# Performance work log

Hardware: AMD Instinct MI355X
Metric: run time of the kernel (lower is better)

The kernel has to match this reference:

```python
import jax, jax.numpy as jnp
import numpy as np

N, E, B = 50000, 800000, 1000
NODE_DIN, BB_DOUT, DHID, K = 32, 64, 64, 3
GLOB_DIN, EMBED_DIN = 64, 64
CIN = BB_DOUT + NODE_DIN  # 96


def setup_inputs() -> dict:
    key = jax.random.key(0)
    ks = jax.random.split(key, 24)

    def w(k, shape, fan_in):
        return jax.random.normal(k, shape, jnp.float32) / np.float32(np.sqrt(fan_in))

    inp = dict(
        x=jax.random.normal(ks[0], (N, NODE_DIN), jnp.float32),
        u=jax.random.normal(ks[1], (B, GLOB_DIN), jnp.float32),
        z=jax.random.normal(ks[2], (N, BB_DOUT), jnp.float32),
        edge_index=jax.random.randint(ks[3], (2, E), 0, N),
        edge_weight=jax.random.uniform(ks[4], (E,), jnp.float32),
        batch=jnp.sort(jax.random.randint(ks[5], (N,), 0, B)),
        batch_size=B,
        prev_h=jax.random.normal(ks[6], (N, DHID), jnp.float32),
    )
    # six ChebConvs of GConvGRU: x-convs take CIN, h-convs take DHID; all output DHID
    for i, nm in enumerate(["xz", "hz", "xr", "hr", "xh", "hh"]):
        cin = CIN if nm[0] == "x" else DHID
        inp[f"W{nm}"] = w(ks[7 + 2 * i], (K, cin, DHID), cin * K)
        inp[f"b{nm}"] = jnp.zeros((DHID,), jnp.float32)
    inp["Wg"] = w(ks[20], (GLOB_DIN, EMBED_DIN), GLOB_DIN)
    inp["bg"] = jnp.zeros((EMBED_DIN,), jnp.float32)
    return inp


def _cheb(xin, W, b, src, dst, w_norm, n):
    """ChebConv with sym norm, lambda_max=2 -> L_hat = -D^-1/2 A D^-1/2 (diag cancels)."""
    def prop(t):  # L_hat @ t  ([N,C])
        return -jax.ops.segment_sum(w_norm[:, None] * t[src], dst, num_segments=n)

    out = xin @ W[0] + b
    tx_prev = xin
    tx = None
    if W.shape[0] > 1:
        tx = prop(xin)
        out = out + tx @ W[1]
    for k in range(2, W.shape[0]):
        tx_new = 2.0 * prop(tx) - tx_prev
        out = out + tx_new @ W[k]
        tx_prev, tx = tx, tx_new
    return out


def reference(x, u, z, edge_index, edge_weight, batch, batch_size, prev_h,
              Wxz, bxz, Whz, bhz, Wxr, bxr, Whr, bhr, Wxh, bxh, Whh, bhh, Wg, bg):
    n = x.shape[0]
    src, dst = edge_index[0], edge_index[1]
    deg = jax.ops.segment_sum(edge_weight, src, num_segments=n)
    deg_safe = jnp.where(deg > 0, deg, 1.0)
    dinv = jnp.where(deg > 0, jax.lax.rsqrt(deg_safe), 0.0)
    w_norm = dinv[src] * edge_weight * dinv[dst]

    xin = jnp.concatenate([z, x], axis=-1)  # [N, CIN]
    Z = jax.nn.sigmoid(_cheb(xin, Wxz, bxz, src, dst, w_norm, n)
                       + _cheb(prev_h, Whz, bhz, src, dst, w_norm, n))
    R = jax.nn.sigmoid(_cheb(xin, Wxr, bxr, src, dst, w_norm, n)
                       + _cheb(prev_h, Whr, bhr, src, dst, w_norm, n))
    Ht = jnp.tanh(_cheb(xin, Wxh, bxh, src, dst, w_norm, n)
                  + _cheb(prev_h * R, Whh, bhh, src, dst, w_norm, n))
    h = Z * prev_h + (1.0 - Z) * Ht

    graph_emb = jax.ops.segment_sum(z, batch, num_segments=batch_size)  # [B, BB_DOUT]
    global_emb = jax.nn.relu(u @ Wg + bg)                                # [B, EMBED_DIN]
    fused = jnp.concatenate([graph_emb, global_emb], axis=-1)           # [B, 128]
    return fused, h
```

## Files before the change

kernel.cpp:

```cpp
#include <hip/hip_runtime.h>

#define NN 50000
#define EE 800000
#define BB 1000
#define NB 196
#define NR 8
#define RS 6272
#define NC 32
#define CHUNK 25000

typedef unsigned short u16;
typedef __attribute__((ext_vector_type(8))) short bf16x8;
typedef __attribute__((ext_vector_type(4))) float f32x4;

static __device__ __forceinline__ u16 f2b(float f) {
    union { float f; unsigned u; } v;
    v.f = f;
    unsigned r = v.u + 0x7fffu + ((v.u >> 16) & 1u);
    return (u16)(r >> 16);
}

static __device__ __forceinline__ float b2f(short s) {
    union { unsigned u; float f; } c;
    c.u = ((unsigned)(u16)s) << 16;
    return c.f;
}

__global__ __launch_bounds__(512) void k_degcnt_lds(
    const int* __restrict__ src, const int* __restrict__ dst,
    const float* __restrict__ ew, float* __restrict__ deg_p,
    int* __restrict__ cnt_p) {
    __shared__ float sdeg[RS];
    __shared__ int scnt[RS];
    int r = blockIdx.x & (NR - 1);
    int c = blockIdx.x >> 3;
    int base = r * RS;
    for (int i = threadIdx.x; i < RS; i += 512) {
        sdeg[i] = 0.f;
        scnt[i] = 0;
    }
    __syncthreads();
    int e0 = c * CHUNK;
    for (int j = threadIdx.x; j < CHUNK; j += 512) {
        int e = e0 + j;
        int s = src[e], d = dst[e];
        int sl = s - base, dl = d - base;
        if ((unsigned)sl < RS) atomicAdd(&sdeg[sl], ew[e]);
        if ((unsigned)dl < RS) atomicAdd(&scnt[dl], 1);
    }
    __syncthreads();
    int lim = (NN - base < RS) ? (NN - base) : RS;
    for (int i = threadIdx.x; i < lim; i += 512) {
        deg_p[(size_t)c * NN + base + i] = sdeg[i];
        cnt_p[(size_t)c * NN + base + i] = scnt[i];
    }
}

__global__ void k_scan1(const int* __restrict__ cnt_p, int* __restrict__ cnt,
                        int* __restrict__ incl, int* __restrict__ bsum) {
    __shared__ int s[256];
    int i = blockIdx.x * 256 + threadIdx.x;
    int v = 0;
    if (i < NN) {
#pragma unroll
        for (int p = 0; p < NC; p++) v += cnt_p[(size_t)p * NN + i];
        cnt[i] = v;
    }
    s[threadIdx.x] = v;
    __syncthreads();
    for (int off = 1; off < 256; off <<= 1) {
        int t = (threadIdx.x >= off) ? s[threadIdx.x - off] : 0;
        __syncthreads();
        s[threadIdx.x] += t;
        __syncthreads();
    }
    if (i < NN) incl[i] = s[threadIdx.x];
    if (threadIdx.x == 255) bsum[blockIdx.x] = s[255];
}

__global__ void k_scan2(int* __restrict__ bsum) {
    __shared__ int s[256];
    int v = (threadIdx.x < NB) ? bsum[threadIdx.x] : 0;
    s[threadIdx.x] = v;
    __syncthreads();
    for (int off = 1; off < 256; off <<= 1) {
        int t = (threadIdx.x >= off) ? s[threadIdx.x - off] : 0;
        __syncthreads();
        s[threadIdx.x] += t;
        __syncthreads();
    }
    if (threadIdx.x < NB) bsum[threadIdx.x] = s[threadIdx.x];
}

__global__ void k_scan3(const int* __restrict__ incl, const int* __restrict__ cnt,
                        const int* __restrict__ bsum, int* __restrict__ row_ptr,
                        int* __restrict__ cursor, const float* __restrict__ deg_p,
                        float* __restrict__ dinv) {
    int i = blockIdx.x * 256 + threadIdx.x;
    if (i >= NN) return;
    int off = (blockIdx.x > 0) ? bsum[blockIdx.x - 1] : 0;
    int start = off + incl[i] - cnt[i];
    row_ptr[i] = start;
    cursor[i] = start;
    float d = 0.f;
#pragma unroll
    for (int p = 0; p < NC; p++) d += deg_p[(size_t)p * NN + i];
    dinv[i] = d > 0.f ? rsqrtf(d) : 0.f;
}

__global__ void k_scatter(const int* __restrict__ src, const int* __restrict__ dst,
                          const float* __restrict__ ew, const float* __restrict__ dinv,
                          int* __restrict__ cursor, uint2* __restrict__ csr8) {
    int e = blockIdx.x * 256 + threadIdx.x;
    if (e >= EE) return;
    int d = dst[e], s = src[e];
    int pos = atomicAdd(&cursor[d], 1);
    float w = dinv[s] * ew[e] * dinv[d];
    csr8[pos] = make_uint2((unsigned)s, __float_as_uint(w));
}

__global__ void k_build_A(const float* __restrict__ z, const float* __restrict__ x,
                          const float* __restrict__ ph, u16* __restrict__ A) {
    int i = blockIdx.x * 256 + threadIdx.x;
    if (i >= NN * 160) return;
    int n = i / 160, c = i - n * 160;
    float v;
    if (c < 64) v = z[n * 64 + c];
    else if (c < 96) v = x[n * 32 + (c - 64)];
    else v = ph[n * 64 + (c - 96)];
    A[(size_t)n * 480 + c] = f2b(v);
}

__global__ void k_packW_all(const float* __restrict__ Wxz, const float* __restrict__ Wxr,
                            const float* __restrict__ Wxh, const float* __restrict__ Whz,
                            const float* __restrict__ Whr, const float* __restrict__ Whh,
                            u16* __restrict__ Wp, u16* __restrict__ W3p) {
    int idx = blockIdx.x * 256 + threadIdx.x;
    if (idx < 15 * 12 * 512) {
        int j = idx & 7, l = (idx >> 3) & 63;
        int ct = (idx >> 9) % 12, s = (idx >> 9) / 12;
        int k = 32 * s + (l >> 4) * 8 + j;
        int g = ct >> 2;
        int c = 16 * (ct & 3) + (l & 15);
        bool isX;
        int kr;
        if (k < 96)       { isX = true;  kr = k; }
        else if (k < 160) { isX = false; kr = k - 96; }
        else if (k < 256) { isX = true;  kr = 96 + (k - 160); }
        else if (k < 320) { isX = false; kr = 64 + (k - 256); }
        else if (k < 416) { isX = true;  kr = 192 + (k - 320); }
        else              { isX = false; kr = 128 + (k - 416); }
        float val;
        if (isX) {
            const float* W = (g == 0) ? Wxz : ((g == 1) ? Wxr : Wxh);
            val = W[kr * 64 + c];
        } else if (g == 2) {
            val = 0.f;
        } else {
            const float* W = (g == 0) ? Whz : Whr;
            val = W[kr * 64 + c];
        }
        Wp[idx] = f2b(val);
    } else {
        int i2 = idx - 15 * 12 * 512;
        if (i2 >= 6 * 4 * 512) return;
        int j = i2 & 7, l = (i2 >> 3) & 63;
        int ct = (i2 >> 9) & 3, s = i2 >> 11;
        int k = 32 * s + (l >> 4) * 8 + j;
        int ki = k >> 6, kr = k & 63;
        int c = 16 * ct + (l & 15);
        W3p[i2] = f2b(Whh[(ki * 64 + kr) * 64 + c]);
    }
}

template <int C, int SCALE, bool HB, int BS, int OS>
__global__ __launch_bounds__(BS) void k_pull(
    const u16* __restrict__ Abase, int inofs, int baseofs, int outofs,
    const uint2* __restrict__ csr8, const int* __restrict__ row_ptr,
    const int* __restrict__ cnt) {
    constexpr int TPR = C / 8;
    int tid = blockIdx.x * BS + threadIdx.x;
    int r = tid / TPR;
    int c8 = (tid - r * TPR) * 8;
    if (r >= NN) return;
    int s0 = row_ptr[r], n = cnt[r];
    float acc[8] = {0.f, 0.f, 0.f, 0.f, 0.f, 0.f, 0.f, 0.f};
    const u16* in = Abase + inofs + c8;
    uint2 e = (n > 0) ? csr8[s0] : make_uint2(0u, 0u);
    for (int j = 0; j < n; j++) {
        uint2 ec = e;
        if (j + 1 < n) e = csr8[s0 + j + 1];
        float w = __uint_as_float(ec.y);
        bf16x8 v = *(const bf16x8*)(in + (size_t)ec.x * OS);
#pragma unroll
        for (int k = 0; k < 8; k++) acc[k] += w * b2f(v[k]);
    }
    const float sc = -(float)SCALE;
    float o[8];
    if (HB) {
        bf16x8 b = *(const bf16x8*)(Abase + (size_t)r * OS + baseofs + c8);
#pragma unroll
        for (int k = 0; k < 8; k++) o[k] = sc * acc[k] - b2f(b[k]);
    } else {
#pragma unroll
        for (int k = 0; k < 8; k++) o[k] = sc * acc[k];
    }
    bf16x8 p;
#pragma unroll
    for (int k = 0; k < 8; k++) p[k] = (short)f2b(o[k]);
    *(bf16x8*)(const_cast<u16*>(Abase) + (size_t)r * OS + outofs + c8) = p;
}

__global__ __launch_bounds__(256) void k_gates_mfma(
    const u16* __restrict__ A, const u16* __restrict__ Wp,
    const float* __restrict__ bxz, const float* __restrict__ bhz,
    const float* __restrict__ bxr, const float* __restrict__ bhr,
    const float* __restrict__ bxh,
    u16* __restrict__ Zb16, u16* __restrict__ Hx16, u16* __restrict__ A3) {
    int wv = (blockIdx.x * 256 + threadIdx.x) >> 6;
    int lane = threadIdx.x & 63;
    int r0 = wv * 16;
    if (r0 >= NN) return;
    int q = lane >> 4, j0 = lane & 15;

    f32x4 acc[12];
#pragma unroll
    for (int i = 0; i < 12; i++) acc[i] = (f32x4){0.f, 0.f, 0.f, 0.f};

    const u16* arow = A + (size_t)(r0 + j0) * 480 + q * 8;
#pragma unroll
    for (int s = 0; s < 15; s++) {
        bf16x8 a = *(const bf16x8*)(arow + 32 * s);
        const u16* bp = Wp + (size_t)(s * 12) * 512 + lane * 8;
#pragma unroll
        for (int ct = 0; ct < 12; ct++) {
            bf16x8 b = *(const bf16x8*)(bp + ct * 512);
            acc[ct] = __builtin_amdgcn_mfma_f32_16x16x32_bf16(a, b, acc[ct], 0, 0, 0);
        }
    }

#pragma unroll
    for (int ct = 0; ct < 4; ct++) {
        int j = 16 * ct + j0;
        float bz = bxz[j] + bhz[j];
        float br = bxr[j] + bhr[j];
        float bh = bxh[j];
#pragma unroll
        for (int reg = 0; reg < 4; reg++) {
            int r = r0 + q * 4 + reg;
            size_t i = (size_t)r * 64 + j;
            float zp = acc[ct][reg] + bz;
            float rp = acc[ct + 4][reg] + br;
            float hp = acc[ct + 8][reg] + bh;
            float zv = 1.f / (1.f + expf(-zp));
            float rv = 1.f / (1.f + expf(-rp));
            float phv = b2f((short)A[(size_t)r * 480 + 96 + j]);
            Zb16[i] = f2b(zv);
            Hx16[i] = f2b(hp);
            A3[(size_t)r * 192 + j] = f2b(rv * phv);
        }
    }
}

__global__ __launch_bounds__(256) void k_final_mfma(
    const u16* __restrict__ A3, const u16* __restrict__ W3p,
    const float* __restrict__ bhh, const u16* __restrict__ Hx16,
    const u16* __restrict__ Zb16, const u16* __restrict__ A,
    float* __restrict__ outh) {
    int wv = (blockIdx.x * 256 + threadIdx.x) >> 6;
    int lane = threadIdx.x & 63;
    int r0 = wv * 16;
    if (r0 >= NN) return;
    int q = lane >> 4, j0 = lane & 15;

    f32x4 acc[4];
#pragma unroll
    for (int i = 0; i < 4; i++) acc[i] = (f32x4){0.f, 0.f, 0.f, 0.f};

    const u16* arow = A3 + (size_t)(r0 + j0) * 192 + q * 8;
#pragma unroll
    for (int s = 0; s < 6; s++) {
        bf16x8 a = *(const bf16x8*)(arow + 32 * s);
        const u16* bp = W3p + (size_t)(s * 4) * 512 + lane * 8;
#pragma unroll
        for (int ct = 0; ct < 4; ct++) {
            bf16x8 b = *(const bf16x8*)(bp + ct * 512);
            acc[ct] = __builtin_amdgcn_mfma_f32_16x16x32_bf16(a, b, acc[ct], 0, 0, 0);
        }
    }

#pragma unroll
    for (int ct = 0; ct < 4; ct++) {
        int j = 16 * ct + j0;
        float bh = bhh[j];
#pragma unroll
        for (int reg = 0; reg < 4; reg++) {
            int r = r0 + q * 4 + reg;
            size_t i = (size_t)r * 64 + j;
            float ht = tanhf(b2f((short)Hx16[i]) + acc[ct][reg] + bh);
            float zv = b2f((short)Zb16[i]);
            float phv = b2f((short)A[(size_t)r * 480 + 96 + j]);
            outh[i] = zv * phv + (1.f - zv) * ht;
        }
    }
}

__global__ __launch_bounds__(256) void k_tail(
    const float* __restrict__ z, const int* __restrict__ batch,
    const float* __restrict__ u, const float* __restrict__ Wg,
    const float* __restrict__ bg, float* __restrict__ out) {
    int b = (blockIdx.x * 256 + threadIdx.x) >> 6;
    int lane = threadIdx.x & 63;
    if (b >= BB) return;
    int lo = 0, hi = NN;
    while (lo < hi) {
        int m = (lo + hi) >> 1;
        if (batch[m] < b) lo = m + 1; else hi = m;
    }
    int start = lo;
    hi = NN;
    while (lo < hi) {
        int m = (lo + hi) >> 1;
        if (batch[m] < b + 1) lo = m + 1; else hi = m;
    }
    int end = lo;
    float acc = 0.f;
    for (int n = start; n < end; n++) acc += z[(size_t)n * 64 + lane];
    float g = bg[lane];
    const float* ur = u + (size_t)b * 64;
    for (int k = 0; k < 64; k++) g += ur[k] * Wg[k * 64 + lane];
    g = fmaxf(g, 0.f);
    out[(size_t)b * 128 + lane] = acc;
    out[(size_t)b * 128 + 64 + lane] = g;
}

extern "C" void kernel_launch(void* const* d_in, const int* in_sizes, int n_in,
                              void* d_out, int out_size, void* d_ws, size_t ws_size,
                              hipStream_t stream) {
    const float* x  = (const float*)d_in[0];
    const float* u  = (const float*)d_in[1];
    const float* z  = (const float*)d_in[2];
    const int*   ei = (const int*)d_in[3];
    const float* ew = (const float*)d_in[4];
    const int* batch = (const int*)d_in[5];
    const float* ph = (const float*)d_in[7];
    const float *Wxz = (const float*)d_in[8],  *bxz = (const float*)d_in[9];
    const float *Whz = (const float*)d_in[10], *bhz = (const float*)d_in[11];
    const float *Wxr = (const float*)d_in[12], *bxr = (const float*)d_in[13];
    const float *Whr = (const float*)d_in[14], *bhr = (const float*)d_in[15];
    const float *Wxh = (const float*)d_in[16], *bxh = (const float*)d_in[17];
    const float *Whh = (const float*)d_in[18], *bhh = (const float*)d_in[19];
    const float *Wg  = (const float*)d_in[20], *bg  = (const float*)d_in[21];
    const int* src = ei;
    const int* dst = ei + EE;

    char* wsb = (char*)d_ws;
    size_t o = 0;
    auto alloc = [&](size_t bytes) {
        void* p = wsb + o;
        o += (bytes + 255) & ~(size_t)255;
        return p;
    };
    float* deg_p   = (float*)alloc((size_t)NC * NN * 4);
    int*   cnt_p   = (int*)alloc((size_t)NC * NN * 4);
    int*   cnt     = (int*)alloc(NN * 4);
    int*   incl    = (int*)alloc(NN * 4);
    int*   row_ptr = (int*)alloc(NN * 4);
    int*   cursor  = (int*)alloc(NN * 4);
    float* dinv    = (float*)alloc(NN * 4);
    int*   bsum    = (int*)alloc(256 * 4);
    uint2* csr8    = (uint2*)alloc((size_t)EE * 8);
    u16*   Zb16 = (u16*)alloc((size_t)NN * 64 * 2);
    u16*   Hx16 = (u16*)alloc((size_t)NN * 64 * 2);
    u16*   A    = (u16*)alloc((size_t)NN * 480 * 2);
    u16*   A3   = (u16*)alloc((size_t)NN * 192 * 2);
    u16*   Wp   = (u16*)alloc(15 * 12 * 512 * 2);
    u16*   W3p  = (u16*)alloc(6 * 4 * 512 * 2);

    float* outF = (float*)d_out;
    float* outH = outF + (size_t)BB * 128;

    const int BLK = 256;
    const int gE = (EE + BLK - 1) / BLK;
    const int gA = (NN * 160 + BLK - 1) / BLK;
    const int gPull160 = (NN + 15) / 16;
    const int gPull64 = (NN + 31) / 32;
    const int gMFMA = (3125 + 3) / 4;
    const int gPack = (15 * 12 * 512 + 6 * 4 * 512 + BLK - 1) / BLK;

    k_packW_all<<<gPack, BLK, 0, stream>>>(Wxz, Wxr, Wxh, Whz, Whr, Whh, Wp, W3p);
    k_build_A<<<gA, BLK, 0, stream>>>(z, x, ph, A);

    k_degcnt_lds<<<NR * NC, 512, 0, stream>>>(src, dst, ew, deg_p, cnt_p);

    k_scan1<<<NB, 256, 0, stream>>>(cnt_p, cnt, incl, bsum);
    k_scan2<<<1, 256, 0, stream>>>(bsum);
    k_scan3<<<NB, 256, 0, stream>>>(incl, cnt, bsum, row_ptr, cursor, deg_p, dinv);
    k_scatter<<<gE, BLK, 0, stream>>>(src, dst, ew, dinv, cursor, csr8);

    k_pull<160, 1, false, 320, 480><<<gPull160, 320, 0, stream>>>(A, 0, 0, 160, csr8, row_ptr, cnt);
    k_pull<160, 2, true, 320, 480><<<gPull160, 320, 0, stream>>>(A, 160, 0, 320, csr8, row_ptr, cnt);

    k_gates_mfma<<<gMFMA, BLK, 0, stream>>>(A, Wp, bxz, bhz, bxr, bhr, bxh, Zb16, Hx16, A3);

    k_pull<64, 1, false, 256, 192><<<gPull64, 256, 0, stream>>>(A3, 0, 0, 64, csr8, row_ptr, cnt);
    k_pull<64, 2, true, 256, 192><<<gPull64, 256, 0, stream>>>(A3, 64, 0, 128, csr8, row_ptr, cnt);

    k_final_mfma<<<gMFMA, BLK, 0, stream>>>(A3, W3p, bhh, Hx16, Zb16, A, outH);

    k_tail<<<(BB * 64 + BLK - 1) / BLK, BLK, 0, stream>>>(z, batch, u, Wg, bg, outF);
}
```

Baseline: 425.7 us.

## Merge prep kernels, fuse scan passes with grid barrier, widen pull per-thread columns

```diff
diff --git a/kernel.cpp b/kernel.cpp
--- a/kernel.cpp
+++ b/kernel.cpp
@@ -9,6 +9,10 @@
 #define NC 32
 #define CHUNK 25000
 
+#define DEGBLKS (NR * NC)
+#define BUILDBLKS 15625
+#define PACKBLKS 204
+
 typedef unsigned short u16;
 typedef __attribute__((ext_vector_type(8))) short bf16x8;
 typedef __attribute__((ext_vector_type(4))) float f32x4;
@@ -26,44 +30,103 @@
     return c.f;
 }
 
-__global__ __launch_bounds__(512) void k_degcnt_lds(
+__global__ __launch_bounds__(512) void k_front(
     const int* __restrict__ src, const int* __restrict__ dst,
-    const float* __restrict__ ew, float* __restrict__ deg_p,
-    int* __restrict__ cnt_p) {
+    const float* __restrict__ ew, float* __restrict__ deg_p, int* __restrict__ cnt_p,
+    const float* __restrict__ z, const float* __restrict__ x,
+    const float* __restrict__ ph, u16* __restrict__ A,
+    const float* __restrict__ Wxz, const float* __restrict__ Wxr,
+    const float* __restrict__ Wxh, const float* __restrict__ Whz,
+    const float* __restrict__ Whr, const float* __restrict__ Whh,
+    u16* __restrict__ Wp, u16* __restrict__ W3p, int* __restrict__ ctr) {
     __shared__ float sdeg[RS];
     __shared__ int scnt[RS];
-    int r = blockIdx.x & (NR - 1);
-    int c = blockIdx.x >> 3;
-    int base = r * RS;
-    for (int i = threadIdx.x; i < RS; i += 512) {
-        sdeg[i] = 0.f;
-        scnt[i] = 0;
-    }
-    __syncthreads();
-    int e0 = c * CHUNK;
-    for (int j = threadIdx.x; j < CHUNK; j += 512) {
-        int e = e0 + j;
-        int s = src[e], d = dst[e];
-        int sl = s - base, dl = d - base;
-        if ((unsigned)sl < RS) atomicAdd(&sdeg[sl], ew[e]);
-        if ((unsigned)dl < RS) atomicAdd(&scnt[dl], 1);
-    }
-    __syncthreads();
-    int lim = (NN - base < RS) ? (NN - base) : RS;
-    for (int i = threadIdx.x; i < lim; i += 512) {
-        deg_p[(size_t)c * NN + base + i] = sdeg[i];
-        cnt_p[(size_t)c * NN + base + i] = scnt[i];
-    }
-}
-
-__global__ void k_scan1(const int* __restrict__ cnt_p, int* __restrict__ cnt,
-                        int* __restrict__ incl, int* __restrict__ bsum) {
+    int bid = blockIdx.x;
+    if (bid < DEGBLKS) {
+        if (bid == 0 && threadIdx.x == 0) atomicExch(ctr, 0);
+        int r = bid & (NR - 1);
+        int c = bid >> 3;
+        int base = r * RS;
+        for (int i = threadIdx.x; i < RS; i += 512) {
+            sdeg[i] = 0.f;
+            scnt[i] = 0;
+        }
+        __syncthreads();
+        int e0 = c * CHUNK;
+        for (int j = threadIdx.x; j < CHUNK; j += 512) {
+            int e = e0 + j;
+            int s = src[e], d = dst[e];
+            int sl = s - base, dl = d - base;
+            if ((unsigned)sl < RS) atomicAdd(&sdeg[sl], ew[e]);
+            if ((unsigned)dl < RS) atomicAdd(&scnt[dl], 1);
+        }
+        __syncthreads();
+        int lim = (NN - base < RS) ? (NN - base) : RS;
+        for (int i = threadIdx.x; i < lim; i += 512) {
+            deg_p[(size_t)c * NN + base + i] = sdeg[i];
+            cnt_p[(size_t)c * NN + base + i] = scnt[i];
+        }
+    } else if (bid < DEGBLKS + BUILDBLKS) {
+        int i = (bid - DEGBLKS) * 512 + threadIdx.x;
+        int n = i / 160, c = i - n * 160;
+        float v;
+        if (c < 64) v = z[n * 64 + c];
+        else if (c < 96) v = x[n * 32 + (c - 64)];
+        else v = ph[n * 64 + (c - 96)];
+        A[(size_t)n * 480 + c] = f2b(v);
+    } else {
+        int idx = (bid - DEGBLKS - BUILDBLKS) * 512 + threadIdx.x;
+        if (idx < 15 * 12 * 512) {
+            int j = idx & 7, l = (idx >> 3) & 63;
+            int ct = (idx >> 9) % 12, s = (idx >> 9) / 12;
+            int k = 32 * s + (l >> 4) * 8 + j;
+            int g = ct >> 2;
+            int c = 16 * (ct & 3) + (l & 15);
+            bool isX;
+            int kr;
+            if (k < 96)       { isX = true;  kr = k; }
+            else if (k < 160) { isX = false; kr = k - 96; }
+            else if (k < 256) { isX = true;  kr = 96 + (k - 160); }
+            else if (k < 320) { isX = false; kr = 64 + (k - 256); }
+            else if (k < 416) { isX = true;  kr = 192 + (k - 320); }
+            else              { isX = false; kr = 128 + (k - 416); }
+            float val;
+            if (isX) {
+                const float* W = (g == 0) ? Wxz : ((g == 1) ? Wxr : Wxh);
+                val = W[kr * 64 + c];
+            } else if (g == 2) {
+                val = 0.f;
+            } else {
+                const float* W = (g == 0) ? Whz : Whr;
+                val = W[kr * 64 + c];
+            }
+            Wp[idx] = f2b(val);
+        } else {
+            int i2 = idx - 15 * 12 * 512;
+            int j = i2 & 7, l = (i2 >> 3) & 63;
+            int ct = (i2 >> 9) & 3, s = i2 >> 11;
+            int k = 32 * s + (l >> 4) * 8 + j;
+            int ki = k >> 6, kr = k & 63;
+            int c = 16 * ct + (l & 15);
+            W3p[i2] = f2b(Whh[(ki * 64 + kr) * 64 + c]);
+        }
+    }
+}
+
+__global__ __launch_bounds__(256) void k_scan(
+    const int* __restrict__ cnt_p, const float* __restrict__ deg_p,
+    int* __restrict__ cnt, int* __restrict__ row_ptr, int* __restrict__ cursor,
+    float* __restrict__ dinv, int* __restrict__ bsum, int* __restrict__ ctr) {
     __shared__ int s[256];
-    int i = blockIdx.x * 256 + threadIdx.x;
+    int b = blockIdx.x;
+    int i = b * 256 + threadIdx.x;
     int v = 0;
+    float d = 0.f;
     if (i < NN) {
 #pragma unroll
         for (int p = 0; p < NC; p++) v += cnt_p[(size_t)p * NN + i];
+#pragma unroll
+        for (int p = 0; p < NC; p++) d += deg_p[(size_t)p * NN + i];
         cnt[i] = v;
     }
     s[threadIdx.x] = v;
@@ -74,38 +137,29 @@
         s[threadIdx.x] += t;
         __syncthreads();
     }
-    if (i < NN) incl[i] = s[threadIdx.x];
-    if (threadIdx.x == 255) bsum[blockIdx.x] = s[255];
-}
-
-__global__ void k_scan2(int* __restrict__ bsum) {
-    __shared__ int s[256];
-    int v = (threadIdx.x < NB) ? bsum[threadIdx.x] : 0;
-    s[threadIdx.x] = v;
+    int incl = s[threadIdx.x];
+    if (threadIdx.x == 255) atomicExch(&bsum[b], s[255]);
+    __threadfence();
+    if (threadIdx.x == 0) {
+        atomicAdd(ctr, 1);
+        while (atomicAdd(ctr, 0) < NB) __builtin_amdgcn_s_sleep(8);
+    }
     __syncthreads();
-    for (int off = 1; off < 256; off <<= 1) {
-        int t = (threadIdx.x >= off) ? s[threadIdx.x - off] : 0;
+    __threadfence();
+    int pv = (threadIdx.x < b) ? atomicAdd(&bsum[threadIdx.x], 0) : 0;
+    s[threadIdx.x] = pv;
+    __syncthreads();
+    for (int off = 128; off > 0; off >>= 1) {
+        if (threadIdx.x < off) s[threadIdx.x] += s[threadIdx.x + off];
         __syncthreads();
-        s[threadIdx.x] += t;
-        __syncthreads();
-    }
-    if (threadIdx.x < NB) bsum[threadIdx.x] = s[threadIdx.x];
-}
-
-__global__ void k_scan3(const int* __restrict__ incl, const int* __restrict__ cnt,
-                        const int* __restrict__ bsum, int* __restrict__ row_ptr,
-                        int* __restrict__ cursor, const float* __restrict__ deg_p,
-                        float* __restrict__ dinv) {
-    int i = blockIdx.x * 256 + threadIdx.x;
-    if (i >= NN) return;
-    int off = (blockIdx.x > 0) ? bsum[blockIdx.x - 1] : 0;
-    int start = off + incl[i] - cnt[i];
-    row_ptr[i] = start;
-    cursor[i] = start;
-    float d = 0.f;
-#pragma unroll
-    for (int p = 0; p < NC; p++) d += deg_p[(size_t)p * NN + i];
-    dinv[i] = d > 0.f ? rsqrtf(d) : 0.f;
+    }
+    int prefix = s[0];
+    if (i < NN) {
+        int start = prefix + incl - v;
+        row_ptr[i] = start;
+        cursor[i] = start;
+        dinv[i] = d > 0.f ? rsqrtf(d) : 0.f;
+    }
 }
 
 __global__ void k_scatter(const int* __restrict__ src, const int* __restrict__ dst,
@@ -119,96 +173,59 @@
     csr8[pos] = make_uint2((unsigned)s, __float_as_uint(w));
 }
 
-__global__ void k_build_A(const float* __restrict__ z, const float* __restrict__ x,
-                          const float* __restrict__ ph, u16* __restrict__ A) {
-    int i = blockIdx.x * 256 + threadIdx.x;
-    if (i >= NN * 160) return;
-    int n = i / 160, c = i - n * 160;
-    float v;
-    if (c < 64) v = z[n * 64 + c];
-    else if (c < 96) v = x[n * 32 + (c - 64)];
-    else v = ph[n * 64 + (c - 96)];
-    A[(size_t)n * 480 + c] = f2b(v);
-}
-
-__global__ void k_packW_all(const float* __restrict__ Wxz, const float* __restrict__ Wxr,
-                            const float* __restrict__ Wxh, const float* __restrict__ Whz,
-                            const float* __restrict__ Whr, const float* __restrict__ Whh,
-                            u16* __restrict__ Wp, u16* __restrict__ W3p) {
-    int idx = blockIdx.x * 256 + threadIdx.x;
-    if (idx < 15 * 12 * 512) {
-        int j = idx & 7, l = (idx >> 3) & 63;
-        int ct = (idx >> 9) % 12, s = (idx >> 9) / 12;
-        int k = 32 * s + (l >> 4) * 8 + j;
-        int g = ct >> 2;
-        int c = 16 * (ct & 3) + (l & 15);
-        bool isX;
-        int kr;
-        if (k < 96)       { isX = true;  kr = k; }
-        else if (k < 160) { isX = false; kr = k - 96; }
-        else if (k < 256) { isX = true;  kr = 96 + (k - 160); }
-        else if (k < 320) { isX = false; kr = 64 + (k - 256); }
-        else if (k < 416) { isX = true;  kr = 192 + (k - 320); }
-        else              { isX = false; kr = 128 + (k - 416); }
-        float val;
-        if (isX) {
-            const float* W = (g == 0) ? Wxz : ((g == 1) ? Wxr : Wxh);
-            val = W[kr * 64 + c];
-        } else if (g == 2) {
-            val = 0.f;
-        } else {
-            const float* W = (g == 0) ? Whz : Whr;
-            val = W[kr * 64 + c];
-        }
-        Wp[idx] = f2b(val);
-    } else {
-        int i2 = idx - 15 * 12 * 512;
-        if (i2 >= 6 * 4 * 512) return;
-        int j = i2 & 7, l = (i2 >> 3) & 63;
-        int ct = (i2 >> 9) & 3, s = i2 >> 11;
-        int k = 32 * s + (l >> 4) * 8 + j;
-        int ki = k >> 6, kr = k & 63;
-        int c = 16 * ct + (l & 15);
-        W3p[i2] = f2b(Whh[(ki * 64 + kr) * 64 + c]);
-    }
-}
-
 template <int C, int SCALE, bool HB, int BS, int OS>
 __global__ __launch_bounds__(BS) void k_pull(
     const u16* __restrict__ Abase, int inofs, int baseofs, int outofs,
     const uint2* __restrict__ csr8, const int* __restrict__ row_ptr,
     const int* __restrict__ cnt) {
-    constexpr int TPR = C / 8;
+    constexpr int TPR = C / 16;
     int tid = blockIdx.x * BS + threadIdx.x;
     int r = tid / TPR;
-    int c8 = (tid - r * TPR) * 8;
+    int c16 = (tid - r * TPR) * 16;
     if (r >= NN) return;
     int s0 = row_ptr[r], n = cnt[r];
-    float acc[8] = {0.f, 0.f, 0.f, 0.f, 0.f, 0.f, 0.f, 0.f};
-    const u16* in = Abase + inofs + c8;
+    float acc[16];
+#pragma unroll
+    for (int k = 0; k < 16; k++) acc[k] = 0.f;
+    const u16* in = Abase + inofs + c16;
     uint2 e = (n > 0) ? csr8[s0] : make_uint2(0u, 0u);
     for (int j = 0; j < n; j++) {
         uint2 ec = e;
         if (j + 1 < n) e = csr8[s0 + j + 1];
         float w = __uint_as_float(ec.y);
-        bf16x8 v = *(const bf16x8*)(in + (size_t)ec.x * OS);
-#pragma unroll
-        for (int k = 0; k < 8; k++) acc[k] += w * b2f(v[k]);
+        const u16* p = in + (size_t)ec.x * OS;
+        bf16x8 v0 = *(const bf16x8*)(p);
+        bf16x8 v1 = *(const bf16x8*)(p + 8);
+#pragma unroll
+        for (int k = 0; k < 8; k++) {
+            acc[k] += w * b2f(v0[k]);
+            acc[8 + k] += w * b2f(v1[k]);
+        }
     }
     const float sc = -(float)SCALE;
-    float o[8];
+    float o[16];
     if (HB) {
-        bf16x8 b = *(const bf16x8*)(Abase + (size_t)r * OS + baseofs + c8);
-#pragma unroll
-        for (int k = 0; k < 8; k++) o[k] = sc * acc[k] - b2f(b[k]);
+        const u16* bp = Abase + (size_t)r * OS + baseofs + c16;
+        bf16x8 b0 = *(const bf16x8*)(bp);
+        bf16x8 b1 = *(const bf16x8*)(bp + 8);
+#pragma unroll
+        for (int k = 0; k < 8; k++) {
+            o[k] = sc * acc[k] - b2f(b0[k]);
+            o[8 + k] = sc * acc[8 + k] - b2f(b1[k]);
+        }
     } else {
 #pragma unroll
-        for (int k = 0; k < 8; k++) o[k] = sc * acc[k];
-    }
-    bf16x8 p;
-#pragma unroll
-    for (int k = 0; k < 8; k++) p[k] = (short)f2b(o[k]);
-    *(bf16x8*)(const_cast<u16*>(Abase) + (size_t)r * OS + outofs + c8) = p;
+        for (int k = 0; k < 16; k++) o[k] = sc * acc[k];
+    }
+    bf16x8 p0, p1;
+#pragma unroll
+    for (int k = 0; k < 8; k++) {
+        p0[k] = (short)f2b(o[k]);
+        p1[k] = (short)f2b(o[8 + k]);
+    }
+    u16* op = const_cast<u16*>(Abase) + (size_t)r * OS + outofs + c16;
+    *(bf16x8*)(op) = p0;
+    *(bf16x8*)(op + 8) = p1;
 }
 
 __global__ __launch_bounds__(256) void k_gates_mfma(
@@ -262,11 +279,41 @@
     }
 }
 
-__global__ __launch_bounds__(256) void k_final_mfma(
+#define FINBLKS 782
+__global__ __launch_bounds__(256) void k_final_tail(
     const u16* __restrict__ A3, const u16* __restrict__ W3p,
     const float* __restrict__ bhh, const u16* __restrict__ Hx16,
     const u16* __restrict__ Zb16, const u16* __restrict__ A,
-    float* __restrict__ outh) {
+    float* __restrict__ outh,
+    const float* __restrict__ z, const int* __restrict__ batch,
+    const float* __restrict__ u, const float* __restrict__ Wg,
+    const float* __restrict__ bg, float* __restrict__ outF) {
+    if (blockIdx.x >= FINBLKS) {
+        int b = ((blockIdx.x - FINBLKS) * 256 + threadIdx.x) >> 6;
+        int lane = threadIdx.x & 63;
+        if (b >= BB) return;
+        int lo = 0, hi = NN;
+        while (lo < hi) {
+            int m = (lo + hi) >> 1;
+            if (batch[m] < b) lo = m + 1; else hi = m;
+        }
+        int start = lo;
+        hi = NN;
+        while (lo < hi) {
+            int m = (lo + hi) >> 1;
+            if (batch[m] < b + 1) lo = m + 1; else hi = m;
+        }
+        int end = lo;
+        float acc = 0.f;
+        for (int n = start; n < end; n++) acc += z[(size_t)n * 64 + lane];
+        float g = bg[lane];
+        const float* ur = u + (size_t)b * 64;
+        for (int k = 0; k < 64; k++) g += ur[k] * Wg[k * 64 + lane];
+        g = fmaxf(g, 0.f);
+        outF[(size_t)b * 128 + lane] = acc;
+        outF[(size_t)b * 128 + 64 + lane] = g;
+        return;
+    }
     int wv = (blockIdx.x * 256 + threadIdx.x) >> 6;
     int lane = threadIdx.x & 63;
     int r0 = wv * 16;
@@ -303,35 +350,6 @@
             outh[i] = zv * phv + (1.f - zv) * ht;
         }
     }
-}
-
-__global__ __launch_bounds__(256) void k_tail(
-    const float* __restrict__ z, const int* __restrict__ batch,
-    const float* __restrict__ u, const float* __restrict__ Wg,
-    const float* __restrict__ bg, float* __restrict__ out) {
-    int b = (blockIdx.x * 256 + threadIdx.x) >> 6;
-    int lane = threadIdx.x & 63;
-    if (b >= BB) return;
-    int lo = 0, hi = NN;
-    while (lo < hi) {
-        int m = (lo + hi) >> 1;
-        if (batch[m] < b) lo = m + 1; else hi = m;
-    }
-    int start = lo;
-    hi = NN;
-    while (lo < hi) {
-        int m = (lo + hi) >> 1;
-        if (batch[m] < b + 1) lo = m + 1; else hi = m;
-    }
-    int end = lo;
-    float acc = 0.f;
-    for (int n = start; n < end; n++) acc += z[(size_t)n * 64 + lane];
-    float g = bg[lane];
-    const float* ur = u + (size_t)b * 64;
-    for (int k = 0; k < 64; k++) g += ur[k] * Wg[k * 64 + lane];
-    g = fmaxf(g, 0.f);
-    out[(size_t)b * 128 + lane] = acc;
-    out[(size_t)b * 128 + 64 + lane] = g;
 }
 
 extern "C" void kernel_launch(void* const* d_in, const int* in_sizes, int n_in,
@@ -364,11 +382,11 @@
     float* deg_p   = (float*)alloc((size_t)NC * NN * 4);
     int*   cnt_p   = (int*)alloc((size_t)NC * NN * 4);
     int*   cnt     = (int*)alloc(NN * 4);
-    int*   incl    = (int*)alloc(NN * 4);
     int*   row_ptr = (int*)alloc(NN * 4);
     int*   cursor  = (int*)alloc(NN * 4);
     float* dinv    = (float*)alloc(NN * 4);
     int*   bsum    = (int*)alloc(256 * 4);
+    int*   ctr     = (int*)alloc(256);
     uint2* csr8    = (uint2*)alloc((size_t)EE * 8);
     u16*   Zb16 = (u16*)alloc((size_t)NN * 64 * 2);
     u16*   Hx16 = (u16*)alloc((size_t)NN * 64 * 2);
@@ -382,20 +400,17 @@
 
     const int BLK = 256;
     const int gE = (EE + BLK - 1) / BLK;
-    const int gA = (NN * 160 + BLK - 1) / BLK;
-    const int gPull160 = (NN + 15) / 16;
-    const int gPull64 = (NN + 31) / 32;
-    const int gMFMA = (3125 + 3) / 4;
-    const int gPack = (15 * 12 * 512 + 6 * 4 * 512 + BLK - 1) / BLK;
-
-    k_packW_all<<<gPack, BLK, 0, stream>>>(Wxz, Wxr, Wxh, Whz, Whr, Whh, Wp, W3p);
-    k_build_A<<<gA, BLK, 0, stream>>>(z, x, ph, A);
-
-    k_degcnt_lds<<<NR * NC, 512, 0, stream>>>(src, dst, ew, deg_p, cnt_p);
-
-    k_scan1<<<NB, 256, 0, stream>>>(cnt_p, cnt, incl, bsum);
-    k_scan2<<<1, 256, 0, stream>>>(bsum);
-    k_scan3<<<NB, 256, 0, stream>>>(incl, cnt, bsum, row_ptr, cursor, deg_p, dinv);
+    const int gPull160 = (NN + 31) / 32;
+    const int gPull64 = (NN + 63) / 64;
+    const int gMFMA = FINBLKS;
+    const int gTail = (BB * 64 + BLK - 1) / BLK;
+
+    k_front<<<DEGBLKS + BUILDBLKS + PACKBLKS, 512, 0, stream>>>(
+        src, dst, ew, deg_p, cnt_p, z, x, ph, A,
+        Wxz, Wxr, Wxh, Whz, Whr, Whh, Wp, W3p, ctr);
+
+    k_scan<<<NB, 256, 0, stream>>>(cnt_p, deg_p, cnt, row_ptr, cursor, dinv, bsum, ctr);
+
     k_scatter<<<gE, BLK, 0, stream>>>(src, dst, ew, dinv, cursor, csr8);
 
     k_pull<160, 1, false, 320, 480><<<gPull160, 320, 0, stream>>>(A, 0, 0, 160, csr8, row_ptr, cnt);
@@ -406,7 +421,6 @@
     k_pull<64, 1, false, 256, 192><<<gPull64, 256, 0, stream>>>(A3, 0, 0, 64, csr8, row_ptr, cnt);
     k_pull<64, 2, true, 256, 192><<<gPull64, 256, 0, stream>>>(A3, 64, 0, 128, csr8, row_ptr, cnt);
 
-    k_final_mfma<<<gMFMA, BLK, 0, stream>>>(A3, W3p, bhh, Hx16, Zb16, A, outH);
-
-    k_tail<<<(BB * 64 + BLK - 1) / BLK, BLK, 0, stream>>>(z, batch, u, Wg, bg, outF);
-}
+    k_final_tail<<<gMFMA + gTail, BLK, 0, stream>>>(A3, W3p, bhh, Hx16, Zb16, A, outH,
+                                                    z, batch, u, Wg, bg, outF);
+}
```

Measured after the change: 426.6 us. About the same (+0.2%).
